# Kernel optimization log

Hardware: AMD Instinct MI355X
Metric: run time of the kernel (lower is better)

The kernel has to match this reference:

```python
import jax, jax.numpy as jnp
import numpy as np

DIM = 512; LAYERS = 6; K = 15; VOCAB = 32000; B = 2; L = 1024
HID = 1024  # SwiGLU hidden: int(512*2) rounded up to multiple of 64
RANK = 64; BLOCK = 2048; MIX_W = 0.1
UP_DIL = [1, 2, 4, 8, 16, 32]
DN_DIL = UP_DIL[::-1]


def rmsnorm(x, w, eps=1e-6):
    return x * jax.lax.rsqrt(jnp.mean(x * x, axis=-1, keepdims=True) + eps) * w


def dconv(x, w, b, dil):
    # x: [B,D,T]; w: [D,1,K] depthwise; left (causal) padding of (K-1)*dil
    pad = (w.shape[-1] - 1) * dil
    y = jax.lax.conv_general_dilated(
        x, w, window_strides=(1,), padding=[(pad, 0)], rhs_dilation=(dil,),
        dimension_numbers=('NCH', 'OIH', 'NCH'), feature_group_count=x.shape[1])
    return y + b[None, :, None]


def conv_block(x, nw, cw, cb, w1, w2, w3, dil):
    # CausalDilatedConv: RMSNorm -> depthwise causal dilated conv -> silu -> SwiGLU -> +residual
    h = rmsnorm(x, nw)
    h = jax.nn.silu(dconv(jnp.transpose(h, (0, 2, 1)), cw, cb, dil))
    h = jnp.transpose(h, (0, 2, 1))
    h = jnp.einsum('bth,dh->btd',
                   jax.nn.silu(jnp.einsum('btd,hd->bth', h, w1)) * jnp.einsum('btd,hd->bth', h, w3),
                   w2)
    return h + x


def run_stack(x, dils, nw, cw, cb, w1, w2, w3, kp, ki, kd, gnorm):
    integral = x; previous = x; current = x
    for i, d in enumerate(dils):
        if i > 0:
            # PIDGate: step == i >= 1 so max(step,1) == i
            pid = kp[i-1] * current + ki[i-1] * (integral / i) + kd[i-1] * (current - previous)
            cur_in = rmsnorm(jax.nn.silu(pid), gnorm[i-1])
        else:
            cur_in = current
        current = conv_block(cur_in, nw[i], cw[i], cb[i], w1[i], w2[i], w3[i], d)
        previous = current
        integral = integral + current
    return current


def mix(x):
    # CausalMeanPool: x + 0.1 * causal running mean
    counts = jnp.arange(1, x.shape[1] + 1, dtype=x.dtype)[None, :, None]
    return x + MIX_W * jnp.cumsum(x, axis=1) / counts


def sgate(new, old, nw, dw, db, uw, ub):
    h = jax.nn.silu(rmsnorm(new, nw) @ dw.T + db)
    g = jax.nn.sigmoid(h @ uw.T + ub)
    return g * new + (1.0 - g) * old


def setup_inputs() -> dict:
    key = jax.random.key(0)
    ks = iter(jax.random.split(key, 64))
    def nrm(shape, s=0.02):
        return jax.random.normal(next(ks), shape, jnp.float32) * s
    def stack_params(p):
        return {
            p + '_norm_w': jnp.ones((LAYERS, DIM), jnp.float32),
            p + '_conv_w': nrm((LAYERS, DIM, 1, K), 0.1),
            p + '_conv_b': jnp.zeros((LAYERS, DIM), jnp.float32),
            p + '_w1': nrm((LAYERS, HID, DIM)),
            p + '_w2': nrm((LAYERS, DIM, HID)),
            p + '_w3': nrm((LAYERS, HID, DIM)),
            p + '_kp': jnp.full((LAYERS - 1, DIM), 0.5, jnp.float32),
            p + '_ki': jnp.full((LAYERS - 1, DIM), 0.3, jnp.float32),
            p + '_kd': jnp.full((LAYERS - 1, DIM), 0.2, jnp.float32),
            p + '_gnorm': jnp.ones((LAYERS - 1, DIM), jnp.float32),
        }
    inp = {
        'idx': jax.random.randint(next(ks), (B, L), 0, VOCAB),
        'emb': nrm((VOCAB, DIM)),
        'pos': nrm((1, BLOCK, DIM)),
        'emb_norm_w': jnp.ones((DIM,), jnp.float32),
        'token_shift': jnp.full((DIM,), 0.5, jnp.float32),
        'mem_gate_w': jnp.zeros((DIM, DIM), jnp.float32),  # nn.init.zeros_
        'mem_gate_b': nrm((DIM,)),
        'memory_p': jnp.zeros((B, DIM), jnp.float32),  # buffer, zero after reset()
        'sg_norm': jnp.ones((3, DIM), jnp.float32),
        'sg_down_w': nrm((3, RANK, DIM)),
        'sg_down_b': jnp.zeros((3, RANK), jnp.float32),
        'sg_up_w': nrm((3, DIM, RANK)),
        'sg_up_b': jnp.zeros((3, DIM), jnp.float32),
        'final_norm_w': jnp.ones((DIM,), jnp.float32),
    }
    inp.update(stack_params('up'))
    inp.update(stack_params('dn'))
    return inp


def _forward(idx, emb, pos, emb_norm_w, token_shift, mem_gate_w, mem_gate_b, memory_p,
             up_norm_w, up_conv_w, up_conv_b, up_w1, up_w2, up_w3, up_kp, up_ki, up_kd, up_gnorm,
             dn_norm_w, dn_conv_w, dn_conv_b, dn_w1, dn_w2, dn_w3, dn_kp, dn_ki, dn_kd, dn_gnorm,
             sg_norm, sg_down_w, sg_down_b, sg_up_w, sg_up_b, final_norm_w):
    T = idx.shape[1]
    x = emb[idx] + pos[:, :T]
    x = rmsnorm(x, emb_norm_w)
    # dropout is identity at eval time
    # memory injection: token-shift mix + sigmoid-gated persistent P-memory
    shifted = jnp.concatenate(
        [x[:, :1], token_shift * x[:, :-1] + (1.0 - token_shift) * x[:, 1:]], axis=1)
    mem = jax.nn.sigmoid(memory_p @ mem_gate_w.T + mem_gate_b)
    x = shifted + mem[:, None, :]
    initial = x
    up_p = (up_norm_w, up_conv_w, up_conv_b, up_w1, up_w2, up_w3, up_kp, up_ki, up_kd, up_gnorm)
    dn_p = (dn_norm_w, dn_conv_w, dn_conv_b, dn_w1, dn_w2, dn_w3, dn_kp, dn_ki, dn_kd, dn_gnorm)
    up1 = mix(run_stack(x, UP_DIL, *up_p))
    gated1 = sgate(up1, initial, sg_norm[0], sg_down_w[0], sg_down_b[0], sg_up_w[0], sg_up_b[0])
    down = mix(run_stack(gated1, DN_DIL, *dn_p))
    gated2 = sgate(down, initial, sg_norm[1], sg_down_w[1], sg_down_b[1], sg_up_w[1], sg_up_b[1])
    up2 = mix(run_stack(gated2, UP_DIL, *up_p))  # up_stack weights are shared/reused
    output = sgate(up2, gated2, sg_norm[2], sg_down_w[2], sg_down_b[2], sg_up_w[2], sg_up_b[2])
    output = rmsnorm(output, final_norm_w)
    return output @ emb.T  # tied head


def reference(idx, emb, pos, emb_norm_w, token_shift, mem_gate_w, mem_gate_b, memory_p,
              up_norm_w, up_conv_w, up_conv_b, up_w1, up_w2, up_w3, up_kp, up_ki, up_kd, up_gnorm,
              dn_norm_w, dn_conv_w, dn_conv_b, dn_w1, dn_w2, dn_w3, dn_kp, dn_ki, dn_kd, dn_gnorm,
              sg_norm, sg_down_w, sg_down_b, sg_up_w, sg_up_b, final_norm_w):
    return _forward(idx, emb, pos, emb_norm_w, token_shift, mem_gate_w, mem_gate_b, memory_p,
                    up_norm_w, up_conv_w, up_conv_b, up_w1, up_w2, up_w3, up_kp, up_ki, up_kd, up_gnorm,
                    dn_norm_w, dn_conv_w, dn_conv_b, dn_w1, dn_w2, dn_w3, dn_kp, dn_ki, dn_kd, dn_gnorm,
                    sg_norm, sg_down_w, sg_down_b, sg_up_w, sg_up_b, final_norm_w)
```

## Files before the change

### kernel.cpp

```cpp
#include <hip/hip_runtime.h>
#include <math.h>

#define DIM 512
#define NLAYERS 6
#define KSZ 15
#define VOCAB 32000
#define BATCH 2
#define SEQ 1024
#define HIDN 1024
#define RANK 64
#define NTOK (BATCH*SEQ)
#define MIXW 0.1f

typedef unsigned short u16;
typedef _Float16 f16;
typedef _Float16 f16x8 __attribute__((ext_vector_type(8)));
typedef _Float16 f16x4 __attribute__((ext_vector_type(4)));
typedef float  f32x4  __attribute__((ext_vector_type(4)));

__device__ __forceinline__ float sigm(float x){ return 1.f/(1.f+__expf(-x)); }

__device__ __forceinline__ float wred(float v){
  #pragma unroll
  for (int o=32;o>0;o>>=1) v += __shfl_xor(v, o, 64);
  return v;
}

#define MFMA16(a,b,c) __builtin_amdgcn_mfma_f32_16x16x32_f16(a,b,c,0,0,0)

__device__ __forceinline__ void gld16(const f16* g, f16* l){
  __builtin_amdgcn_global_load_lds(
      (const __attribute__((address_space(1))) void*)g,
      (__attribute__((address_space(3))) void*)l, 16, 0, 0);
}

template<int N> __device__ __forceinline__ void vwait(){
  asm volatile("s_waitcnt vmcnt(%0)" :: "i"(N) : "memory");
}
__device__ __forceinline__ void pipe_bar(){
  __builtin_amdgcn_s_barrier();
  __builtin_amdgcn_sched_barrier(0);
}
#define SBAR() __builtin_amdgcn_sched_barrier(0)

__global__ __launch_bounds__(256) void k_cvt(const float* __restrict__ s,
    f16* __restrict__ d, long n4){
  long i = (long)blockIdx.x*256 + threadIdx.x;
  if (i >= n4) return;
  float4 v = reinterpret_cast<const float4*>(s)[i];
  f16x4 o; o.x=(f16)v.x; o.y=(f16)v.y; o.z=(f16)v.z; o.w=(f16)v.w;
  reinterpret_cast<f16x4*>(d)[i] = o;
}

__global__ __launch_bounds__(256) void k_cvtconv(const float* __restrict__ cw,
    float* __restrict__ cwT, int n){
  int i = blockIdx.x*256 + threadIdx.x;
  if (i >= n) return;
  int d = i & (DIM-1); int m = (i >> 9) % KSZ; int l = i / (KSZ*DIM);
  cwT[i] = cw[((size_t)l*DIM + d)*KSZ + (KSZ-1-m)];
}

__global__ __launch_bounds__(64) void k_embnorm(const int* __restrict__ idx,
    const float* __restrict__ emb, const float* __restrict__ pos,
    const float* __restrict__ w, float* __restrict__ out){
  int row = blockIdx.x;
  int t = row & (SEQ-1);
  int lane = threadIdx.x;
  long ebase = (long)idx[row]*DIM;
  long pbase = (long)t*DIM;
  float v[8]; float ss = 0.f;
  #pragma unroll
  for (int c=0;c<2;c++){
    int d = c*256 + lane*4;
    float4 e = *reinterpret_cast<const float4*>(emb + ebase + d);
    float4 p = *reinterpret_cast<const float4*>(pos + pbase + d);
    float x0 = e.x+p.x, x1 = e.y+p.y, x2 = e.z+p.z, x3 = e.w+p.w;
    v[c*4+0]=x0; v[c*4+1]=x1; v[c*4+2]=x2; v[c*4+3]=x3;
    ss += x0*x0 + x1*x1 + x2*x2 + x3*x3;
  }
  ss = wred(ss);
  float rs = rsqrtf(ss*(1.f/DIM) + 1e-6f);
  long ob = (long)row*DIM;
  #pragma unroll
  for (int c=0;c<2;c++){
    int d = c*256 + lane*4;
    float4 wv = *reinterpret_cast<const float4*>(w + d);
    float4 o;
    o.x = v[c*4+0]*rs*wv.x; o.y = v[c*4+1]*rs*wv.y;
    o.z = v[c*4+2]*rs*wv.z; o.w = v[c*4+3]*rs*wv.w;
    *reinterpret_cast<float4*>(out + ob + d) = o;
  }
}

__global__ void k_mem(const float* __restrict__ p, const float* __restrict__ gw,
                      const float* __restrict__ gb, float* __restrict__ mem){
  int i = blockIdx.x*blockDim.x + threadIdx.x;
  if (i >= BATCH*DIM) return;
  int b = i >> 9, d = i & (DIM-1);
  float acc = gb[d];
  const float* wr = gw + (long)d*DIM;
  const float* pr = p + b*DIM;
  for (int k=0;k<DIM;k+=4){
    float4 wv = *reinterpret_cast<const float4*>(wr+k);
    float4 pv = *reinterpret_cast<const float4*>(pr+k);
    acc += wv.x*pv.x + wv.y*pv.y + wv.z*pv.z + wv.w*pv.w;
  }
  mem[i] = sigm(acc);
}

__global__ void k_shift(const float* __restrict__ xn, const float* __restrict__ mem,
    const float* __restrict__ ts, float* __restrict__ out){
  int i = blockIdx.x*256 + threadIdx.x;
  int d = i & (DIM-1); int row = i >> 9; int t = row & (SEQ-1); int b = row >> 10;
  float cur = xn[i];
  float v;
  if (t == 0) v = cur;
  else { float f = ts[d]; v = f*xn[i-DIM] + (1.f-f)*cur; }
  out[i] = v + mem[b*DIM + d];
}

__global__ __launch_bounds__(64) void k_rms(const float* __restrict__ x,
    const float* __restrict__ w, f16* __restrict__ oh){
  int row = blockIdx.x; int lane = threadIdx.x;
  const float* xr = x + (long)row*DIM;
  float v[8]; float ss = 0.f;
  #pragma unroll
  for (int c=0;c<2;c++){
    int d = c*256 + lane*4;
    float4 f = *reinterpret_cast<const float4*>(xr + d);
    v[c*4+0]=f.x; v[c*4+1]=f.y; v[c*4+2]=f.z; v[c*4+3]=f.w;
    ss += f.x*f.x + f.y*f.y + f.z*f.z + f.w*f.w;
  }
  ss = wred(ss);
  float rs = rsqrtf(ss*(1.f/DIM) + 1e-6f);
  long ob = (long)row*DIM;
  #pragma unroll
  for (int c=0;c<2;c++){
    int d = c*256 + lane*4;
    float4 wv = *reinterpret_cast<const float4*>(w + d);
    f16x4 o;
    o.x = (f16)(v[c*4+0]*rs*wv.x); o.y = (f16)(v[c*4+1]*rs*wv.y);
    o.z = (f16)(v[c*4+2]*rs*wv.z); o.w = (f16)(v[c*4+3]*rs*wv.w);
    *reinterpret_cast<f16x4*>(oh + ob + d) = o;
  }
}

__global__ __launch_bounds__(64) void k_pid(const float* __restrict__ C,
    const float* __restrict__ I, float inv_i,
    const float* __restrict__ kp, const float* __restrict__ ki,
    const float* __restrict__ gn, const float* __restrict__ nw,
    float* __restrict__ xin, f16* __restrict__ oh){
  int row = blockIdx.x; int lane = threadIdx.x;
  long base = (long)row*DIM;
  float u[8]; float ss = 0.f;
  #pragma unroll
  for (int c=0;c<2;c++){
    int d = c*256 + lane*4;
    float4 cv = *reinterpret_cast<const float4*>(C + base + d);
    float4 iv = *reinterpret_cast<const float4*>(I + base + d);
    float4 kpv = *reinterpret_cast<const float4*>(kp + d);
    float4 kiv = *reinterpret_cast<const float4*>(ki + d);
    float p0 = kpv.x*cv.x + kiv.x*(iv.x*inv_i);
    float p1 = kpv.y*cv.y + kiv.y*(iv.y*inv_i);
    float p2 = kpv.z*cv.z + kiv.z*(iv.z*inv_i);
    float p3 = kpv.w*cv.w + kiv.w*(iv.w*inv_i);
    float s0 = p0*sigm(p0), s1 = p1*sigm(p1), s2 = p2*sigm(p2), s3 = p3*sigm(p3);
    u[c*4+0]=s0; u[c*4+1]=s1; u[c*4+2]=s2; u[c*4+3]=s3;
    ss += s0*s0 + s1*s1 + s2*s2 + s3*s3;
  }
  ss = wred(ss);
  float rs1 = rsqrtf(ss*(1.f/DIM) + 1e-6f);
  float x2[8]; float ss2 = 0.f;
  #pragma unroll
  for (int c=0;c<2;c++){
    int d = c*256 + lane*4;
    float4 gv = *reinterpret_cast<const float4*>(gn + d);
    float y0 = u[c*4+0]*rs1*gv.x, y1 = u[c*4+1]*rs1*gv.y;
    float y2 = u[c*4+2]*rs1*gv.z, y3 = u[c*4+3]*rs1*gv.w;
    x2[c*4+0]=y0; x2[c*4+1]=y1; x2[c*4+2]=y2; x2[c*4+3]=y3;
    ss2 += y0*y0 + y1*y1 + y2*y2 + y3*y3;
    float4 o; o.x=y0; o.y=y1; o.z=y2; o.w=y3;
    *reinterpret_cast<float4*>(xin + base + d) = o;
  }
  ss2 = wred(ss2);
  float rs2 = rsqrtf(ss2*(1.f/DIM) + 1e-6f);
  #pragma unroll
  for (int c=0;c<2;c++){
    int d = c*256 + lane*4;
    float4 nv = *reinterpret_cast<const float4*>(nw + d);
    f16x4 o;
    o.x = (f16)(x2[c*4+0]*rs2*nv.x); o.y = (f16)(x2[c*4+1]*rs2*nv.y);
    o.z = (f16)(x2[c*4+2]*rs2*nv.z); o.w = (f16)(x2[c*4+3]*rs2*nv.w);
    *reinterpret_cast<f16x4*>(oh + base + d) = o;
  }
}

__global__ __launch_bounds__(256) void k_conv(const f16* __restrict__ h1,
    const float* __restrict__ cwT, const float* __restrict__ cb,
    f16* __restrict__ hc, int dil){
  int i = blockIdx.x*256 + threadIdx.x;
  int d8 = (i & 63) << 3; int row = i >> 6; int t = row & (SEQ-1);
  float acc[8];
  {
    float4 b0 = *reinterpret_cast<const float4*>(&cb[d8]);
    float4 b1 = *reinterpret_cast<const float4*>(&cb[d8+4]);
    acc[0]=b0.x; acc[1]=b0.y; acc[2]=b0.z; acc[3]=b0.w;
    acc[4]=b1.x; acc[5]=b1.y; acc[6]=b1.z; acc[7]=b1.w;
  }
  #pragma unroll
  for (int m=0;m<KSZ;m++){
    if (t - m*dil >= 0){
      f16x8 h = *reinterpret_cast<const f16x8*>(&h1[(size_t)(row - m*dil)*DIM + d8]);
      float4 w0 = *reinterpret_cast<const float4*>(&cwT[m*DIM + d8]);
      float4 w1 = *reinterpret_cast<const float4*>(&cwT[m*DIM + d8 + 4]);
      acc[0]+=w0.x*(float)h[0]; acc[1]+=w0.y*(float)h[1];
      acc[2]+=w0.z*(float)h[2]; acc[3]+=w0.w*(float)h[3];
      acc[4]+=w1.x*(float)h[4]; acc[5]+=w1.y*(float)h[5];
      acc[6]+=w1.z*(float)h[6]; acc[7]+=w1.w*(float)h[7];
    }
  }
  f16x8 o;
  #pragma unroll
  for (int j=0;j<8;j++){ o[j] = (f16)(acc[j]*sigm(acc[j])); }
  *reinterpret_cast<f16x8*>(&hc[(size_t)row*DIM + d8]) = o;
}


__global__ __launch_bounds__(256) void k_dual(const f16* __restrict__ A,
    const f16* __restrict__ W1, const f16* __restrict__ W3, f16* __restrict__ G){
  __shared__ __align__(16) f16 smem[4*8192];
  int tid = threadIdx.x, lane = tid&63, wid = tid>>6;
  int m0 = blockIdx.x*64, n0 = blockIdx.y*64;
  int r16 = lane&15, kq = lane>>4;
  const f16* arow = A + (size_t)(m0 + wid*16 + r16)*512;

  f16x8 areg[3][2];
#define DALOAD(B,T) { \
    areg[B][0] = *reinterpret_cast<const f16x8*>(arow + (T)*64 + (0*4+kq)*8); \
    areg[B][1] = *reinterpret_cast<const f16x8*>(arow + (T)*64 + (1*4+kq)*8); }

  auto stage = [&](int buf, int t){
    #pragma unroll
    for (int j=0;j<4;j++){
      int cc = j*256 + tid;
      int mat = cc>>9, c2 = cc&511, r = c2>>3, s = c2&7;
      const f16* src = (mat ? W3 : W1) + (size_t)(n0+r)*512 + t*64 + ((s^(r&7))<<3);
      gld16(src, smem + buf*8192 + (j*256 + wid*64)*8);
    }
  };
  f32x4 a1[4] = {}, a3[4] = {};
#define DCOMP(T) { \
    const f16* sbt = smem + ((T)&3)*8192; \
    _Pragma("unroll") \
    for (int kk=0;kk<2;kk++){ \
      int kp0 = kk*4 + kq; \
      _Pragma("unroll") \
      for (int nf=0;nf<4;nf++){ \
        int row = nf*16 + r16; \
        f16x8 b1 = *reinterpret_cast<const f16x8*>(&sbt[row*64 + ((kp0^(row&7))<<3)]); \
        f16x8 b3 = *reinterpret_cast<const f16x8*>(&sbt[4096 + row*64 + ((kp0^(row&7))<<3)]); \
        a1[nf] = MFMA16(areg[(T)%3][kk], b1, a1[nf]); \
        a3[nf] = MFMA16(areg[(T)%3][kk], b3, a3[nf]); \
      } \
    } }
  DALOAD(0,0); DALOAD(1,1); SBAR();
  stage(0,0); SBAR(); stage(1,1); SBAR(); stage(2,2);
#define DITER(T,NW) { vwait<NW>(); pipe_bar(); \
    if ((T)+2 < 8) DALOAD(((T)+2)%3, (T)+2); \
    if ((T)+3 < 8) stage(((T)+3)&3, (T)+3); \
    DCOMP(T); }
  DITER(0,8) DITER(1,10) DITER(2,6) DITER(3,6) DITER(4,6) DITER(5,6) DITER(6,2) DITER(7,0)
#undef DITER
#undef DCOMP
#undef DALOAD
  __syncthreads();
  float* stg = (float*)smem + wid*1088;
  int dr = (lane>>4)*4, dc = lane&15;
  #pragma unroll
  for (int nf=0;nf<4;nf++)
    #pragma unroll
    for (int q=0;q<4;q++){
      float x1 = a1[nf][q];
      stg[(dr+q)*68 + nf*16 + dc] = x1*sigm(x1)*a3[nf][q];
    }
  int gmb = m0 + wid*16;
  #pragma unroll
  for (int pass=0;pass<2;pass++){
    int rr = pass*8 + (lane>>3), c = 8*(lane&7);
    float4 lo = *reinterpret_cast<float4*>(&stg[rr*68 + c]);
    float4 hi = *reinterpret_cast<float4*>(&stg[rr*68 + c + 4]);
    f16x8 o;
    o[0]=(f16)lo.x; o[1]=(f16)lo.y; o[2]=(f16)lo.z; o[3]=(f16)lo.w;
    o[4]=(f16)hi.x; o[5]=(f16)hi.y; o[6]=(f16)hi.z; o[7]=(f16)hi.w;
    *reinterpret_cast<f16x8*>(&G[(size_t)(gmb+rr)*HIDN + n0 + c]) = o;
  }
}

__global__ __launch_bounds__(256) void k_w2(const f16* __restrict__ A,
    const f16* __restrict__ W, const float* __restrict__ XIN,
    float* __restrict__ OF, float* __restrict__ I, int init){
  __shared__ __align__(16) f16 smem[4*4096];
  int tid = threadIdx.x, lane = tid&63, wid = tid>>6;
  int m0 = blockIdx.x*64, n0 = blockIdx.y*32;
  int r16 = lane&15, kq = lane>>4;
  const f16* arow = A + (size_t)(m0 + wid*16 + r16)*1024;

  f16x8 areg[3][4];
#define WALOAD(B,T) { \
    areg[B][0] = *reinterpret_cast<const f16x8*>(arow + (T)*128 + (0*4+kq)*8); \
    areg[B][1] = *reinterpret_cast<const f16x8*>(arow + (T)*128 + (1*4+kq)*8); \
    areg[B][2] = *reinterpret_cast<const f16x8*>(arow + (T)*128 + (2*4+kq)*8); \
    areg[B][3] = *reinterpret_cast<const f16x8*>(arow + (T)*128 + (3*4+kq)*8); }

  auto stage = [&](int buf, int t){
    #pragma unroll
    for (int j=0;j<2;j++){
      int cc = j*256 + tid;
      int r = cc>>4, s = cc&15;
      int g = (s&8) | ((s^(r&7))&7);
      const f16* src = W + (size_t)(n0+r)*1024 + t*128 + (g<<3);
      gld16(src, smem + buf*4096 + (j*256 + wid*64)*8);
    }
  };
  f32x4 acc[2] = {};
#define WCOMP(T) { \
    const f16* sbt = smem + ((T)&3)*4096; \
    _Pragma("unroll") \
    for (int kk=0;kk<4;kk++){ \
      int kp0 = kk*4 + kq; \
      _Pragma("unroll") \
      for (int nf=0;nf<2;nf++){ \
        int row = nf*16 + r16; \
        int sl = (kp0&8) | ((kp0^(row&7))&7); \
        f16x8 bv = *reinterpret_cast<const f16x8*>(&sbt[row*128 + (sl<<3)]); \
        acc[nf] = MFMA16(areg[(T)%3][kk], bv, acc[nf]); \
      } \
    } }
  WALOAD(0,0); WALOAD(1,1); SBAR();
  stage(0,0); SBAR(); stage(1,1); SBAR(); stage(2,2);
#define WITER(T,NW) { vwait<NW>(); pipe_bar(); \
    if ((T)+2 < 8) WALOAD(((T)+2)%3, (T)+2); \
    if ((T)+3 < 8) stage(((T)+3)&3, (T)+3); \
    WCOMP(T); }
  WITER(0,4) WITER(1,8) WITER(2,6) WITER(3,6) WITER(4,6) WITER(5,6) WITER(6,4) WITER(7,0)
#undef WITER
#undef WCOMP
#undef WALOAD
  __syncthreads();
  float* stg = (float*)smem + wid*(16*36);
  int dr = (lane>>4)*4, dc = lane&15;
  #pragma unroll
  for (int nf=0;nf<2;nf++)
    #pragma unroll
    for (int q=0;q<4;q++)
      stg[(dr+q)*36 + nf*16 + dc] = acc[nf][q];
  int gmb = m0 + wid*16;
  #pragma unroll
  for (int pass=0;pass<2;pass++){
    int rr = pass*8 + (lane>>3), c = 4*(lane&7);
    float4 v = *reinterpret_cast<float4*>(&stg[rr*36 + c]);
    size_t o = (size_t)(gmb+rr)*DIM + n0 + c;
    float4 x = *reinterpret_cast<const float4*>(&XIN[o]);
    v.x+=x.x; v.y+=x.y; v.z+=x.z; v.w+=x.w;
    *reinterpret_cast<float4*>(&OF[o]) = v;
    float4 iv;
    if (init) iv = x;
    else      iv = *reinterpret_cast<const float4*>(&I[o]);
    iv.x+=v.x; iv.y+=v.y; iv.z+=v.z; iv.w+=v.w;
    *reinterpret_cast<float4*>(&I[o]) = iv;
  }
}

__global__ __launch_bounds__(512) void k_logits(const f16* __restrict__ A,
    const f16* __restrict__ E, float* __restrict__ OF){
  __shared__ __align__(16) char smemc[34816];
  f16* sB = (f16*)smemc;
  int tid = threadIdx.x, lane = tid&63, wid = tid>>6;
  int bid = blockIdx.x;
  int m0 = (bid&7)*256, n0 = (bid>>3)*64;
  int r16 = lane&15, kq = lane>>4;
  const f16* arow0 = A + (size_t)(m0 + wid*32 +      r16)*512;
  const f16* arow1 = A + (size_t)(m0 + wid*32 + 16 + r16)*512;

  f16x8 areg[3][2][2];
#define LALOAD(B,T) { \
    areg[B][0][0] = *reinterpret_cast<const f16x8*>(arow0 + (T)*64 + (0*4+kq)*8); \
    areg[B][0][1] = *reinterpret_cast<const f16x8*>(arow0 + (T)*64 + (1*4+kq)*8); \
    areg[B][1][0] = *reinterpret_cast<const f16x8*>(arow1 + (T)*64 + (0*4+kq)*8); \
    areg[B][1][1] = *reinterpret_cast<const f16x8*>(arow1 + (T)*64 + (1*4+kq)*8); }

  auto stage = [&](int buf, int t){
    int cc = tid;
    int r = cc>>3, s = cc&7;
    gld16(E + (size_t)(n0+r)*512 + t*64 + ((s^(r&7))<<3), sB + buf*4096 + wid*64*8);
  };
  f32x4 acc[2][4] = {};
#define LCOMP(T) { \
    const f16* sbt = sB + ((T)&3)*4096; \
    _Pragma("unroll") \
    for (int kk=0;kk<2;kk++){ \
      int kp0 = kk*4 + kq; \
      _Pragma("unroll") \
      for (int nf=0;nf<4;nf++){ \
        int row = nf*16 + r16; \
        f16x8 bv = *reinterpret_cast<const f16x8*>(&sbt[row*64 + ((kp0^(row&7))<<3)]); \
        acc[0][nf] = MFMA16(areg[(T)%3][0][kk], bv, acc[0][nf]); \
        acc[1][nf] = MFMA16(areg[(T)%3][1][kk], bv, acc[1][nf]); \
      } \
    } }
  LALOAD(0,0); LALOAD(1,1); SBAR();
  stage(0,0); SBAR(); stage(1,1); SBAR(); stage(2,2);
#define LITER(T,NW) { vwait<NW>(); pipe_bar(); \
    if ((T)+2 < 8) LALOAD(((T)+2)%3, (T)+2); \
    if ((T)+3 < 8) stage(((T)+3)&3, (T)+3); \
    LCOMP(T); }
  LITER(0,2) LITER(1,6) LITER(2,5) LITER(3,5) LITER(4,5) LITER(5,5) LITER(6,4) LITER(7,0)
#undef LITER
#undef LCOMP
#undef LALOAD
  __syncthreads();
  int dr = (lane>>4)*4, dc = lane&15;
  float* stg = (float*)smemc + wid*1088;
  #pragma unroll
  for (int mf=0;mf<2;mf++){
    #pragma unroll
    for (int nf=0;nf<4;nf++)
      #pragma unroll
      for (int q=0;q<4;q++)
        stg[(dr+q)*68 + nf*16 + dc] = acc[mf][nf][q];
    int gmb = m0 + wid*32 + mf*16;
    #pragma unroll
    for (int pass=0;pass<4;pass++){
      int rr = pass*4 + (lane>>4), c = 4*(lane&15);
      float4 v = *reinterpret_cast<float4*>(&stg[rr*68 + c]);
      *reinterpret_cast<float4*>(&OF[(size_t)(gmb+rr)*VOCAB + n0 + c]) = v;
    }
  }
}

__global__ __launch_bounds__(64) void k_mix(float* __restrict__ x){
  int col = blockIdx.x;
  int b = col >> 9, d = col & (DIM-1);
  int lane = threadIdx.x;
  long o = (long)b*SEQ*DIM + d + (long)lane*16*DIM;
  float v[16]; float s = 0.f;
  #pragma unroll
  for (int j=0;j<16;j++){ v[j] = x[o + (long)j*DIM]; s += v[j]; }
  float t = s;
  #pragma unroll
  for (int off=1; off<64; off<<=1){
    float u = __shfl_up(t, off, 64);
    if (lane >= off) t += u;
  }
  float run = t - s;
  #pragma unroll
  for (int j=0;j<16;j++){
    run += v[j];
    int tt = lane*16 + j;
    x[o + (long)j*DIM] = v[j] + MIXW*run/(float)(tt+1);
  }
}

__global__ __launch_bounds__(256) void k_sgate(const float* __restrict__ xnew,
    const float* __restrict__ xold, const float* __restrict__ nw,
    const float* __restrict__ dw, const float* __restrict__ db,
    const float* __restrict__ uw, const float* __restrict__ ub,
    float* __restrict__ out){
  __shared__ float raw[DIM];
  __shared__ float xn[DIM];
  __shared__ float part[256];
  __shared__ float hb[RANK];
  int row = blockIdx.x, tid = threadIdx.x;
  long base = (long)row*DIM;
  float ss = 0.f;
  for (int d=tid; d<DIM; d+=256){ float v = xnew[base+d]; raw[d]=v; ss += v*v; }
  ss = wred(ss);
  if ((tid&63)==0) part[tid>>6] = ss;
  __syncthreads();
  float tot = part[0]+part[1]+part[2]+part[3];
  float rs = rsqrtf(tot*(1.f/DIM)+1e-6f);
  for (int d=tid; d<DIM; d+=256) xn[d] = raw[d]*rs*nw[d];
  __syncthreads();
  int rr = tid & 63, q = tid >> 6;
  float p = 0.f;
  const float* dwr = dw + (long)rr*DIM + q*128;
  const float* xq = xn + q*128;
  #pragma unroll 8
  for (int d=0; d<128; d+=4){
    float4 wv = *reinterpret_cast<const float4*>(dwr+d);
    p += xq[d]*wv.x + xq[d+1]*wv.y + xq[d+2]*wv.z + xq[d+3]*wv.w;
  }
  part[tid] = p;
  __syncthreads();
  if (tid < RANK){
    float h = part[tid] + part[64+tid] + part[128+tid] + part[192+tid] + db[tid];
    hb[tid] = h * sigm(h);
  }
  __syncthreads();
  for (int d=tid; d<DIM; d+=256){
    float a = ub[d];
    const float* ur = uw + (long)d*RANK;
    #pragma unroll
    for (int rj=0;rj<RANK;rj+=4){
      float4 uv = *reinterpret_cast<const float4*>(ur+rj);
      a += hb[rj]*uv.x + hb[rj+1]*uv.y + hb[rj+2]*uv.z + hb[rj+3]*uv.w;
    }
    float g = sigm(a);
    out[base+d] = g*raw[d] + (1.f-g)*xold[base+d];
  }
}

extern "C" void kernel_launch(void* const* d_in, const int* in_sizes, int n_in,
                              void* d_out, int out_size, void* d_ws, size_t ws_size,
                              hipStream_t stream){
  const int*   idx           = (const int*)d_in[0];
  const float* emb           = (const float*)d_in[1];
  const float* pos           = (const float*)d_in[2];
  const float* emb_norm_w    = (const float*)d_in[3];
  const float* token_shift   = (const float*)d_in[4];
  const float* mem_gate_w    = (const float*)d_in[5];
  const float* mem_gate_b    = (const float*)d_in[6];
  const float* memory_p      = (const float*)d_in[7];
  const float* sg_norm       = (const float*)d_in[8];
  const float* sg_down_w     = (const float*)d_in[9];
  const float* sg_down_b     = (const float*)d_in[10];
  const float* sg_up_w       = (const float*)d_in[11];
  const float* sg_up_b       = (const float*)d_in[12];
  const float* final_norm_w  = (const float*)d_in[13];
  struct StackP { const float *nw, *cw, *cb, *w1, *w2, *w3, *kp, *ki, *gn; };
  StackP up { (const float*)d_in[14], (const float*)d_in[15], (const float*)d_in[16],
              (const float*)d_in[17], (const float*)d_in[18], (const float*)d_in[19],
              (const float*)d_in[20], (const float*)d_in[21], (const float*)d_in[23] };
  StackP dn { (const float*)d_in[24], (const float*)d_in[25], (const float*)d_in[26],
              (const float*)d_in[27], (const float*)d_in[28], (const float*)d_in[29],
              (const float*)d_in[30], (const float*)d_in[31], (const float*)d_in[33] };

  char* wp = (char*)d_ws;
  auto alloc = [&](size_t bytes)->void*{
    void* p = (void*)wp; wp += (bytes + 255) & ~(size_t)255; return p;
  };
  float* A0  = (float*)alloc((size_t)NTOK*DIM*4);
  float* A1  = (float*)alloc((size_t)NTOK*DIM*4);
  float* Cb  = (float*)alloc((size_t)NTOK*DIM*4);
  float* Ib  = (float*)alloc((size_t)NTOK*DIM*4);
  float* XIN = (float*)alloc((size_t)NTOK*DIM*4);
  f16*   H1  = (f16*)alloc((size_t)NTOK*DIM*2);
  f16*   HC  = (f16*)alloc((size_t)NTOK*DIM*2);
  f16*   G   = (f16*)alloc((size_t)NTOK*HIDN*2);
  const size_t WSZ = (size_t)NLAYERS*HIDN*DIM;
  f16*   UpW1 = (f16*)alloc(WSZ*2);
  f16*   UpW2 = (f16*)alloc(WSZ*2);
  f16*   UpW3 = (f16*)alloc(WSZ*2);
  f16*   DnW1 = (f16*)alloc(WSZ*2);
  f16*   DnW2 = (f16*)alloc(WSZ*2);
  f16*   DnW3 = (f16*)alloc(WSZ*2);
  f16*   Ef   = (f16*)alloc((size_t)VOCAB*DIM*2);
  float* UpCT = (float*)alloc((size_t)NLAYERS*KSZ*DIM*4);
  float* DnCT = (float*)alloc((size_t)NLAYERS*KSZ*DIM*4);
  float* MEM  = (float*)alloc((size_t)BATCH*DIM*4);

  static const int updil[NLAYERS] = {1,2,4,8,16,32};
  static const int dndil[NLAYERS] = {32,16,8,4,2,1};

  {
    long n4 = WSZ/4;
    int g = (int)((n4 + 255)/256);
    k_cvt<<<g,256,0,stream>>>(up.w1, UpW1, n4);
    k_cvt<<<g,256,0,stream>>>(up.w2, UpW2, n4);
    k_cvt<<<g,256,0,stream>>>(up.w3, UpW3, n4);
    k_cvt<<<g,256,0,stream>>>(dn.w1, DnW1, n4);
    k_cvt<<<g,256,0,stream>>>(dn.w2, DnW2, n4);
    k_cvt<<<g,256,0,stream>>>(dn.w3, DnW3, n4);
    long e4 = (long)VOCAB*DIM/4;
    k_cvt<<<(int)((e4+255)/256),256,0,stream>>>(emb, Ef, e4);
    int nc = NLAYERS*KSZ*DIM;
    k_cvtconv<<<(nc+255)/256,256,0,stream>>>(up.cw, UpCT, nc);
    k_cvtconv<<<(nc+255)/256,256,0,stream>>>(dn.cw, DnCT, nc);
  }

  k_embnorm<<<NTOK,64,0,stream>>>(idx, emb, pos, emb_norm_w, Cb);
  k_mem<<<(BATCH*DIM+255)/256,256,0,stream>>>(memory_p, mem_gate_w, mem_gate_b, MEM);
  k_shift<<<NTOK*DIM/256,256,0,stream>>>(Cb, MEM, token_shift, A0);

  auto run_stack = [&](const float* xs, const StackP& S, const float* CT,
                       const f16* W1f, const f16* W2f, const f16* W3f, const int* dil){
    for (int l=0;l<NLAYERS;l++){
      const float* bin;
      if (l==0){
        bin = xs;
        k_rms<<<NTOK,64,0,stream>>>(xs, S.nw + l*DIM, H1);
      } else {
        k_pid<<<NTOK,64,0,stream>>>(Cb, Ib, 1.f/(float)l,
            S.kp+(l-1)*DIM, S.ki+(l-1)*DIM, S.gn+(l-1)*DIM, S.nw+l*DIM, XIN, H1);
        bin = XIN;
      }
      k_conv<<<NTOK*DIM/8/256,256,0,stream>>>(H1, CT + (size_t)l*KSZ*DIM, S.cb + l*DIM, HC, dil[l]);
      k_dual<<<dim3(NTOK/64, HIDN/64),256,0,stream>>>(
          HC, W1f + (size_t)l*HIDN*DIM, W3f + (size_t)l*HIDN*DIM, G);
      k_w2<<<dim3(NTOK/64, DIM/32),256,0,stream>>>(
          G, W2f + (size_t)l*DIM*HIDN, bin, Cb, Ib, (l==0)?1:0);
    }
  };

  run_stack(A0, up, UpCT, UpW1, UpW2, UpW3, updil);
  k_mix<<<BATCH*DIM,64,0,stream>>>(Cb);
  k_sgate<<<NTOK,256,0,stream>>>(Cb, A0, sg_norm, sg_down_w, sg_down_b, sg_up_w, sg_up_b, A1);
  run_stack(A1, dn, DnCT, DnW1, DnW2, DnW3, dndil);
  k_mix<<<BATCH*DIM,64,0,stream>>>(Cb);
  k_sgate<<<NTOK,256,0,stream>>>(Cb, A0, sg_norm+DIM, sg_down_w+RANK*DIM, sg_down_b+RANK,
                                 sg_up_w+DIM*RANK, sg_up_b+DIM, A1);
  run_stack(A1, up, UpCT, UpW1, UpW2, UpW3, updil);
  k_mix<<<BATCH*DIM,64,0,stream>>>(Cb);
  k_sgate<<<NTOK,256,0,stream>>>(Cb, A1, sg_norm+2*DIM, sg_down_w+2*RANK*DIM, sg_down_b+2*RANK,
                                 sg_up_w+2*DIM*RANK, sg_up_b+2*DIM, Cb);
  k_rms<<<NTOK,64,0,stream>>>(Cb, final_norm_w, H1);
  k_logits<<<8*(VOCAB/64),512,0,stream>>>(H1, Ef, (float*)d_out);
}
```

Measured before the change: 1.126 ms.

## Retile GEMM pipelines: narrower dual tile, deeper-K logits stages, double-buffered A regs

k_dual now uses a 32-wide N tile, so it launches twice as many blocks with half the shared memory and fewer accumulators. In k_dual, k_w2 and k_logits, the A-register prefetch drops from three buffers to two, and a barrier is added after each A load. k_logits moves to 128-wide K stages with triple-buffered shared memory and 4 iterations, changing its swizzle and vmcnt waits. The aim is better occupancy and fewer pipeline steps, at the cost of extra barriers and less prefetch distance.

```diff
diff --git a/kernel.cpp b/kernel.cpp
--- a/kernel.cpp
+++ b/kernel.cpp
@@ -228,67 +228,66 @@
 
 __global__ __launch_bounds__(256) void k_dual(const f16* __restrict__ A,
     const f16* __restrict__ W1, const f16* __restrict__ W3, f16* __restrict__ G){
-  __shared__ __align__(16) f16 smem[4*8192];
+  __shared__ __align__(16) f16 smem[4*4096];
   int tid = threadIdx.x, lane = tid&63, wid = tid>>6;
-  int m0 = blockIdx.x*64, n0 = blockIdx.y*64;
+  int m0 = blockIdx.x*64, n0 = blockIdx.y*32;
   int r16 = lane&15, kq = lane>>4;
   const f16* arow = A + (size_t)(m0 + wid*16 + r16)*512;
 
-  f16x8 areg[3][2];
+  f16x8 areg[2][2];
 #define DALOAD(B,T) { \
     areg[B][0] = *reinterpret_cast<const f16x8*>(arow + (T)*64 + (0*4+kq)*8); \
     areg[B][1] = *reinterpret_cast<const f16x8*>(arow + (T)*64 + (1*4+kq)*8); }
 
   auto stage = [&](int buf, int t){
     #pragma unroll
-    for (int j=0;j<4;j++){
+    for (int j=0;j<2;j++){
       int cc = j*256 + tid;
-      int mat = cc>>9, c2 = cc&511, r = c2>>3, s = c2&7;
+      int mat = cc>>8, c2 = cc&255, r = c2>>3, s = c2&7;
       const f16* src = (mat ? W3 : W1) + (size_t)(n0+r)*512 + t*64 + ((s^(r&7))<<3);
-      gld16(src, smem + buf*8192 + (j*256 + wid*64)*8);
+      gld16(src, smem + buf*4096 + cc*8);
     }
   };
-  f32x4 a1[4] = {}, a3[4] = {};
+  f32x4 a1[2] = {}, a3[2] = {};
 #define DCOMP(T) { \
-    const f16* sbt = smem + ((T)&3)*8192; \
+    const f16* sbt = smem + ((T)&3)*4096; \
     _Pragma("unroll") \
     for (int kk=0;kk<2;kk++){ \
       int kp0 = kk*4 + kq; \
       _Pragma("unroll") \
-      for (int nf=0;nf<4;nf++){ \
+      for (int nf=0;nf<2;nf++){ \
         int row = nf*16 + r16; \
         f16x8 b1 = *reinterpret_cast<const f16x8*>(&sbt[row*64 + ((kp0^(row&7))<<3)]); \
-        f16x8 b3 = *reinterpret_cast<const f16x8*>(&sbt[4096 + row*64 + ((kp0^(row&7))<<3)]); \
-        a1[nf] = MFMA16(areg[(T)%3][kk], b1, a1[nf]); \
-        a3[nf] = MFMA16(areg[(T)%3][kk], b3, a3[nf]); \
+        f16x8 b3 = *reinterpret_cast<const f16x8*>(&sbt[2048 + row*64 + ((kp0^(row&7))<<3)]); \
+        a1[nf] = MFMA16(areg[(T)&1][kk], b1, a1[nf]); \
+        a3[nf] = MFMA16(areg[(T)&1][kk], b3, a3[nf]); \
       } \
     } }
-  DALOAD(0,0); DALOAD(1,1); SBAR();
+  DALOAD(0,0); SBAR();
   stage(0,0); SBAR(); stage(1,1); SBAR(); stage(2,2);
 #define DITER(T,NW) { vwait<NW>(); pipe_bar(); \
-    if ((T)+2 < 8) DALOAD(((T)+2)%3, (T)+2); \
+    if ((T)+1 < 8) DALOAD(((T)+1)&1, (T)+1); SBAR(); \
     if ((T)+3 < 8) stage(((T)+3)&3, (T)+3); \
     DCOMP(T); }
-  DITER(0,8) DITER(1,10) DITER(2,6) DITER(3,6) DITER(4,6) DITER(5,6) DITER(6,2) DITER(7,0)
+  DITER(0,4) DITER(1,2) DITER(2,2) DITER(3,2) DITER(4,2) DITER(5,2) DITER(6,0) DITER(7,0)
 #undef DITER
 #undef DCOMP
 #undef DALOAD
   __syncthreads();
-  float* stg = (float*)smem + wid*1088;
+  float* stg = (float*)smem + wid*576;
   int dr = (lane>>4)*4, dc = lane&15;
   #pragma unroll
-  for (int nf=0;nf<4;nf++)
+  for (int nf=0;nf<2;nf++)
     #pragma unroll
     for (int q=0;q<4;q++){
       float x1 = a1[nf][q];
-      stg[(dr+q)*68 + nf*16 + dc] = x1*sigm(x1)*a3[nf][q];
+      stg[(dr+q)*36 + nf*16 + dc] = x1*sigm(x1)*a3[nf][q];
     }
   int gmb = m0 + wid*16;
-  #pragma unroll
-  for (int pass=0;pass<2;pass++){
-    int rr = pass*8 + (lane>>3), c = 8*(lane&7);
-    float4 lo = *reinterpret_cast<float4*>(&stg[rr*68 + c]);
-    float4 hi = *reinterpret_cast<float4*>(&stg[rr*68 + c + 4]);
+  {
+    int rr = lane>>2, c = 8*(lane&3);
+    float4 lo = *reinterpret_cast<float4*>(&stg[rr*36 + c]);
+    float4 hi = *reinterpret_cast<float4*>(&stg[rr*36 + c + 4]);
     f16x8 o;
     o[0]=(f16)lo.x; o[1]=(f16)lo.y; o[2]=(f16)lo.z; o[3]=(f16)lo.w;
     o[4]=(f16)hi.x; o[5]=(f16)hi.y; o[6]=(f16)hi.z; o[7]=(f16)hi.w;
@@ -305,7 +304,7 @@
   int r16 = lane&15, kq = lane>>4;
   const f16* arow = A + (size_t)(m0 + wid*16 + r16)*1024;
 
-  f16x8 areg[3][4];
+  f16x8 areg[2][4];
 #define WALOAD(B,T) { \
     areg[B][0] = *reinterpret_cast<const f16x8*>(arow + (T)*128 + (0*4+kq)*8); \
     areg[B][1] = *reinterpret_cast<const f16x8*>(arow + (T)*128 + (1*4+kq)*8); \
@@ -319,7 +318,7 @@
       int r = cc>>4, s = cc&15;
       int g = (s&8) | ((s^(r&7))&7);
       const f16* src = W + (size_t)(n0+r)*1024 + t*128 + (g<<3);
-      gld16(src, smem + buf*4096 + (j*256 + wid*64)*8);
+      gld16(src, smem + buf*4096 + cc*8);
     }
   };
   f32x4 acc[2] = {};
@@ -333,21 +332,21 @@
         int row = nf*16 + r16; \
         int sl = (kp0&8) | ((kp0^(row&7))&7); \
         f16x8 bv = *reinterpret_cast<const f16x8*>(&sbt[row*128 + (sl<<3)]); \
-        acc[nf] = MFMA16(areg[(T)%3][kk], bv, acc[nf]); \
+        acc[nf] = MFMA16(areg[(T)&1][kk], bv, acc[nf]); \
       } \
     } }
-  WALOAD(0,0); WALOAD(1,1); SBAR();
+  WALOAD(0,0); SBAR();
   stage(0,0); SBAR(); stage(1,1); SBAR(); stage(2,2);
 #define WITER(T,NW) { vwait<NW>(); pipe_bar(); \
-    if ((T)+2 < 8) WALOAD(((T)+2)%3, (T)+2); \
+    if ((T)+1 < 8) WALOAD(((T)+1)&1, (T)+1); SBAR(); \
     if ((T)+3 < 8) stage(((T)+3)&3, (T)+3); \
     WCOMP(T); }
-  WITER(0,4) WITER(1,8) WITER(2,6) WITER(3,6) WITER(4,6) WITER(5,6) WITER(6,4) WITER(7,0)
+  WITER(0,4) WITER(1,2) WITER(2,2) WITER(3,2) WITER(4,2) WITER(5,2) WITER(6,0) WITER(7,0)
 #undef WITER
 #undef WCOMP
 #undef WALOAD
   __syncthreads();
-  float* stg = (float*)smem + wid*(16*36);
+  float* stg = (float*)smem + wid*576;
   int dr = (lane>>4)*4, dc = lane&15;
   #pragma unroll
   for (int nf=0;nf<2;nf++)
@@ -373,8 +372,7 @@
 
 __global__ __launch_bounds__(512) void k_logits(const f16* __restrict__ A,
     const f16* __restrict__ E, float* __restrict__ OF){
-  __shared__ __align__(16) char smemc[34816];
-  f16* sB = (f16*)smemc;
+  __shared__ __align__(16) f16 sB[3*8192];
   int tid = threadIdx.x, lane = tid&63, wid = tid>>6;
   int bid = blockIdx.x;
   int m0 = (bid&7)*256, n0 = (bid>>3)*64;
@@ -382,45 +380,51 @@
   const f16* arow0 = A + (size_t)(m0 + wid*32 +      r16)*512;
   const f16* arow1 = A + (size_t)(m0 + wid*32 + 16 + r16)*512;
 
-  f16x8 areg[3][2][2];
+  f16x8 areg[2][2][4];
 #define LALOAD(B,T) { \
-    areg[B][0][0] = *reinterpret_cast<const f16x8*>(arow0 + (T)*64 + (0*4+kq)*8); \
-    areg[B][0][1] = *reinterpret_cast<const f16x8*>(arow0 + (T)*64 + (1*4+kq)*8); \
-    areg[B][1][0] = *reinterpret_cast<const f16x8*>(arow1 + (T)*64 + (0*4+kq)*8); \
-    areg[B][1][1] = *reinterpret_cast<const f16x8*>(arow1 + (T)*64 + (1*4+kq)*8); }
+    _Pragma("unroll") \
+    for (int kk=0;kk<4;kk++){ \
+      areg[B][0][kk] = *reinterpret_cast<const f16x8*>(arow0 + (T)*128 + (kk*4+kq)*8); \
+      areg[B][1][kk] = *reinterpret_cast<const f16x8*>(arow1 + (T)*128 + (kk*4+kq)*8); \
+    } }
 
   auto stage = [&](int buf, int t){
-    int cc = tid;
-    int r = cc>>3, s = cc&7;
-    gld16(E + (size_t)(n0+r)*512 + t*64 + ((s^(r&7))<<3), sB + buf*4096 + wid*64*8);
+    #pragma unroll
+    for (int j=0;j<2;j++){
+      int cc = j*512 + tid;
+      int r = cc>>4, s = cc&15;
+      int g = (s&8) | ((s^(r&7))&7);
+      gld16(E + (size_t)(n0+r)*512 + t*128 + (g<<3), sB + buf*8192 + cc*8);
+    }
   };
   f32x4 acc[2][4] = {};
 #define LCOMP(T) { \
-    const f16* sbt = sB + ((T)&3)*4096; \
+    const f16* sbt = sB + ((T)%3)*8192; \
     _Pragma("unroll") \
-    for (int kk=0;kk<2;kk++){ \
+    for (int kk=0;kk<4;kk++){ \
       int kp0 = kk*4 + kq; \
       _Pragma("unroll") \
       for (int nf=0;nf<4;nf++){ \
         int row = nf*16 + r16; \
-        f16x8 bv = *reinterpret_cast<const f16x8*>(&sbt[row*64 + ((kp0^(row&7))<<3)]); \
-        acc[0][nf] = MFMA16(areg[(T)%3][0][kk], bv, acc[0][nf]); \
-        acc[1][nf] = MFMA16(areg[(T)%3][1][kk], bv, acc[1][nf]); \
+        int sl = (kp0&8) | ((kp0^(row&7))&7); \
+        f16x8 bv = *reinterpret_cast<const f16x8*>(&sbt[row*128 + (sl<<3)]); \
+        acc[0][nf] = MFMA16(areg[(T)&1][0][kk], bv, acc[0][nf]); \
+        acc[1][nf] = MFMA16(areg[(T)&1][1][kk], bv, acc[1][nf]); \
       } \
     } }
-  LALOAD(0,0); LALOAD(1,1); SBAR();
-  stage(0,0); SBAR(); stage(1,1); SBAR(); stage(2,2);
+  LALOAD(0,0); SBAR();
+  stage(0,0); SBAR(); stage(1,1);
 #define LITER(T,NW) { vwait<NW>(); pipe_bar(); \
-    if ((T)+2 < 8) LALOAD(((T)+2)%3, (T)+2); \
-    if ((T)+3 < 8) stage(((T)+3)&3, (T)+3); \
+    if ((T)+1 < 4) LALOAD(((T)+1)&1, (T)+1); SBAR(); \
+    if ((T)+2 < 4) stage(((T)+2)%3, (T)+2); \
     LCOMP(T); }
-  LITER(0,2) LITER(1,6) LITER(2,5) LITER(3,5) LITER(4,5) LITER(5,5) LITER(6,4) LITER(7,0)
+  LITER(0,2) LITER(1,2) LITER(2,2) LITER(3,0)
 #undef LITER
 #undef LCOMP
 #undef LALOAD
   __syncthreads();
   int dr = (lane>>4)*4, dc = lane&15;
-  float* stg = (float*)smemc + wid*1088;
+  float* stg = (float*)sB + wid*1088;
   #pragma unroll
   for (int mf=0;mf<2;mf++){
     #pragma unroll
@@ -595,7 +599,7 @@
         bin = XIN;
       }
       k_conv<<<NTOK*DIM/8/256,256,0,stream>>>(H1, CT + (size_t)l*KSZ*DIM, S.cb + l*DIM, HC, dil[l]);
-      k_dual<<<dim3(NTOK/64, HIDN/64),256,0,stream>>>(
+      k_dual<<<dim3(NTOK/64, HIDN/32),256,0,stream>>>(
           HC, W1f + (size_t)l*HIDN*DIM, W3f + (size_t)l*HIDN*DIM, G);
       k_w2<<<dim3(NTOK/64, DIM/32),256,0,stream>>>(
           G, W2f + (size_t)l*DIM*HIDN, bin, Cb, Ib, (l==0)?1:0);
```

Result: slower. 1.177 ms (+4.5%).
